# Kernel tuning notes

Hardware: AMD Instinct MI355X
Metric: run time of the kernel (lower is better)

## Reference

```python
import jax, jax.numpy as jnp
import numpy as np

N = 50000
E = 300000
NEG_SLOPE = 0.2
EPS = 1e-16


def setup_inputs() -> dict:
    key = jax.random.key(0)
    ks = jax.random.split(key, 12)
    x = jax.random.normal(ks[0], (N, 27), dtype=jnp.float32)
    edge_index = jax.random.randint(ks[1], (2, E), 0, N, dtype=jnp.int64)
    # layer 1: in=27 -> heads1=4, dim=64
    W1 = jax.random.normal(ks[2], (27, 4 * 64), dtype=jnp.float32) * 0.1
    a_src1 = jax.random.normal(ks[3], (4, 64), dtype=jnp.float32) * 0.1
    a_dst1 = jax.random.normal(ks[4], (4, 64), dtype=jnp.float32) * 0.1
    b1 = jnp.zeros((4 * 64,), dtype=jnp.float32)
    # layer 2: in=256 -> heads2=2, dim=64
    W2 = jax.random.normal(ks[5], (256, 2 * 64), dtype=jnp.float32) * 0.05
    a_src2 = jax.random.normal(ks[6], (2, 64), dtype=jnp.float32) * 0.1
    a_dst2 = jax.random.normal(ks[7], (2, 64), dtype=jnp.float32) * 0.1
    b2 = jnp.zeros((2 * 64,), dtype=jnp.float32)
    # final linear: 128 -> 1
    Wfc = jax.random.normal(ks[8], (128, 1), dtype=jnp.float32) * 0.05
    bfc = jnp.zeros((1,), dtype=jnp.float32)
    return {"x": x, "edge_index": edge_index, "W1": W1, "a_src1": a_src1,
            "a_dst1": a_dst1, "b1": b1, "W2": W2, "a_src2": a_src2,
            "a_dst2": a_dst2, "b2": b2, "Wfc": Wfc, "bfc": bfc}


def gat_layer(x, src, dst, W, a_src, a_dst, b, heads, dim):
    # h: [N, H, D]
    h = (x @ W).reshape(N, heads, dim)
    # per-node attention half-scores: [N, H]
    s_src = jnp.einsum('nhd,hd->nh', h, a_src)
    s_dst = jnp.einsum('nhd,hd->nh', h, a_dst)
    # per-edge logits (gather) + leaky relu: [E', H]
    logits = jax.nn.leaky_relu(s_src[src] + s_dst[dst], negative_slope=NEG_SLOPE)
    # segment softmax over incoming edges at each destination node
    m = jax.ops.segment_max(logits, dst, num_segments=N)  # [N, H]
    m = jnp.where(jnp.isfinite(m), m, 0.0)
    e = jnp.exp(logits - m[dst])
    z = jax.ops.segment_sum(e, dst, num_segments=N)  # [N, H]
    alpha = e / (z[dst] + EPS)
    # weighted scatter-aggregate of source features
    out = jax.ops.segment_sum(h[src] * alpha[:, :, None], dst, num_segments=N)
    return out.reshape(N, heads * dim) + b


def reference(x, edge_index, W1, a_src1, a_dst1, b1, W2, a_src2, a_dst2, b2, Wfc, bfc):
    # add self-loops (PyG GATConv default add_self_loops=True)
    loops = jnp.arange(N, dtype=edge_index.dtype)
    src = jnp.concatenate([edge_index[0], loops])
    dst = jnp.concatenate([edge_index[1], loops])
    h = gat_layer(x, src, dst, W1, a_src1, a_dst1, b1, heads=4, dim=64)
    h = jax.nn.elu(h)
    h = gat_layer(h, src, dst, W2, a_src2, a_dst2, b2, heads=2, dim=64)
    h = jax.nn.elu(h)
    out = h @ Wfc + bfc
    return jax.nn.sigmoid(out)
```

## Files before the change

### kernel.cpp

```cpp
#include <hip/hip_runtime.h>
#include <math.h>

#define N_NODES 50000
#define N_PAD   50016
#define E_EDGES 300000
#define E_TOT   350000
#define NEG 0.2f
#define EPS 1e-16f
#define CAP 32

typedef __attribute__((ext_vector_type(8))) short bf16x8;
typedef __attribute__((ext_vector_type(4))) float f32x4;

__device__ __forceinline__ float leaky(float x) { return x > 0.f ? x : NEG * x; }
__device__ __forceinline__ short f2bf(float v) {
    unsigned u = __float_as_uint(v);
    u += 0x7fffu + ((u >> 16) & 1u);
    return (short)(u >> 16);
}
__device__ __forceinline__ float bflo(unsigned u) { return __uint_as_float(u << 16); }
__device__ __forceinline__ float bfhi(unsigned u) { return __uint_as_float(u & 0xffff0000u); }
__device__ __forceinline__ unsigned bfpack(short a, short b) {
    return (unsigned)(unsigned short)a | ((unsigned)(unsigned short)b << 16);
}

__global__ __launch_bounds__(256) void k_scatter_s1(const int* __restrict__ ei,
        int* __restrict__ cnt, int* __restrict__ eidx,
        const float* __restrict__ x,
        const float* __restrict__ W1, const float* __restrict__ as1,
        const float* __restrict__ ad1, const float* __restrict__ W2,
        float* __restrict__ s1, short* __restrict__ rec,
        short* __restrict__ W1b, short* __restrict__ W2bT) {
    __shared__ float wsvL[216];
    int t = blockIdx.x * 256 + threadIdx.x;
    if (threadIdx.x < 216) {
        int k = threadIdx.x >> 3, j = threadIdx.x & 7;
        const float* av = (j < 4) ? (as1 + j * 64) : (ad1 + (j - 4) * 64);
        const float* wr = W1 + k * 256 + ((j & 3) * 64);
        float s = 0.f;
        #pragma unroll
        for (int d = 0; d < 64; ++d) s += wr[d] * av[d];
        wsvL[threadIdx.x] = s;
    }
    if (t < E_TOT) {
        int s = (t < E_EDGES) ? ei[t] : (t - E_EDGES);
        int d = (t < E_EDGES) ? ei[E_EDGES + t] : (t - E_EDGES);
        int pos = atomicAdd(&cnt[d], 1);
        if (pos < CAP) eidx[d * CAP + pos] = s;
    }
    if (t < 32768) {
        int col = t >> 8, k = t & 255;
        W2bT[t] = f2bf(W2[k * 128 + col]);
    }
    if (t < 8192) {
        int h = t >> 11, col = (t >> 5) & 63, k = t & 31;
        W1b[t] = f2bf(k < 27 ? W1[k * 256 + h * 64 + col] : 0.f);
    }
    __syncthreads();
    if (t < N_NODES * 8) {
        int n = t >> 3, j = t & 7;
        float s = 0.f;
        #pragma unroll
        for (int k = 0; k < 27; ++k) s += x[n * 27 + k] * wsvL[k * 8 + j];
        s1[t] = s;
        if (j < 4) ((float*)rec)[n * 32 + j] = s;
        int c0 = j * 4;
        short p0 = f2bf(c0 + 0 < 27 ? x[n * 27 + c0 + 0] : 0.f);
        short p1 = f2bf(c0 + 1 < 27 ? x[n * 27 + c0 + 1] : 0.f);
        short p2 = f2bf(c0 + 2 < 27 ? x[n * 27 + c0 + 2] : 0.f);
        short p3 = f2bf(c0 + 3 < 27 ? x[n * 27 + c0 + 3] : 0.f);
        uint2 wv;
        wv.x = bfpack(p0, p1);
        wv.y = bfpack(p2, p3);
        *(uint2*)(rec + n * 64 + 8 + c0) = wv;
    }
}

__global__ __launch_bounds__(256) void k_gd(const int* __restrict__ cnt,
        const int* __restrict__ eidx, const short* __restrict__ rec,
        const float* __restrict__ s1, const short* __restrict__ W1b,
        const short* __restrict__ W2bT, const float* __restrict__ b1,
        const float* __restrict__ as2, const float* __restrict__ ad2,
        short* __restrict__ h2b, float* __restrict__ s2) {
    __shared__ short XA[4][32][32];
    __shared__ short O[32 * 264];
    __shared__ float P[4][2][32];
    const float* recf = (const float*)rec;
    int n0 = blockIdx.x * 32;
    f32x4 z4 = {0.f, 0.f, 0.f, 0.f};

    {
        int g = threadIdx.x >> 4;
        int q = threadIdx.x & 15;
        int c2 = 2 * q;
        #pragma unroll
        for (int p = 0; p < 2; ++p) {
            int m = p * 16 + g;
            int n = n0 + m;
            if (n >= N_NODES) {
                *(unsigned*)&XA[0][m][c2] = 0u;
                *(unsigned*)&XA[1][m][c2] = 0u;
                *(unsigned*)&XA[2][m][c2] = 0u;
                *(unsigned*)&XA[3][m][c2] = 0u;
                continue;
            }
            int beg = n * CAP;
            int deg = min(cnt[n], CAP);
            float4 sdv = *(const float4*)(s1 + n * 8 + 4);
            float a0 = 0.f, a1 = 0.f, a2 = 0.f, a3 = 0.f;
            float b0 = 0.f, b1v = 0.f, b2v = 0.f, b3 = 0.f;
            float z0 = 0.f, z1 = 0.f, z2 = 0.f, z3 = 0.f;
            int last = beg + deg - 1;
            for (int i = 0; i < deg; i += 4) {
                bool m1 = (i + 1) < deg, m2 = (i + 2) < deg, m3 = (i + 3) < deg;
                int p0 = beg + i;
                int p1 = m1 ? p0 + 1 : last;
                int p2 = m2 ? p0 + 2 : last;
                int p3 = m3 ? p0 + 3 : last;
                int s0 = eidx[p0];
                int s1i = eidx[p1];
                int s2i = eidx[p2];
                int s3 = eidx[p3];
                float4 sv0 = *(const float4*)(recf + s0 * 32);
                float4 sv1 = *(const float4*)(recf + s1i * 32);
                float4 sv2 = *(const float4*)(recf + s2i * 32);
                float4 sv3 = *(const float4*)(recf + s3 * 32);
                unsigned xv0 = *(const unsigned*)(rec + s0 * 64 + 8 + c2);
                unsigned xv1 = *(const unsigned*)(rec + s1i * 64 + 8 + c2);
                unsigned xv2 = *(const unsigned*)(rec + s2i * 64 + 8 + c2);
                unsigned xv3 = *(const unsigned*)(rec + s3 * 64 + 8 + c2);
                float xa0 = bflo(xv0), xc0 = bfhi(xv0);
                float xa1 = bflo(xv1), xc1 = bfhi(xv1);
                float xa2 = bflo(xv2), xc2 = bfhi(xv2);
                float xa3 = bflo(xv3), xc3 = bfhi(xv3);
                float g1 = m1 ? 1.f : 0.f, g2 = m2 ? 1.f : 0.f, g3 = m3 ? 1.f : 0.f;
                float e00 = __expf(leaky(sv0.x + sdv.x));
                float e01 = __expf(leaky(sv0.y + sdv.y));
                float e02 = __expf(leaky(sv0.z + sdv.z));
                float e03 = __expf(leaky(sv0.w + sdv.w));
                float e10 = g1 * __expf(leaky(sv1.x + sdv.x));
                float e11 = g1 * __expf(leaky(sv1.y + sdv.y));
                float e12 = g1 * __expf(leaky(sv1.z + sdv.z));
                float e13 = g1 * __expf(leaky(sv1.w + sdv.w));
                float e20 = g2 * __expf(leaky(sv2.x + sdv.x));
                float e21 = g2 * __expf(leaky(sv2.y + sdv.y));
                float e22 = g2 * __expf(leaky(sv2.z + sdv.z));
                float e23 = g2 * __expf(leaky(sv2.w + sdv.w));
                float e30 = g3 * __expf(leaky(sv3.x + sdv.x));
                float e31 = g3 * __expf(leaky(sv3.y + sdv.y));
                float e32 = g3 * __expf(leaky(sv3.z + sdv.z));
                float e33 = g3 * __expf(leaky(sv3.w + sdv.w));
                z0 += e00 + e10 + e20 + e30;
                z1 += e01 + e11 + e21 + e31;
                z2 += e02 + e12 + e22 + e32;
                z3 += e03 + e13 + e23 + e33;
                a0 += e00 * xa0 + e10 * xa1 + e20 * xa2 + e30 * xa3;
                a1 += e01 * xa0 + e11 * xa1 + e21 * xa2 + e31 * xa3;
                a2 += e02 * xa0 + e12 * xa1 + e22 * xa2 + e32 * xa3;
                a3 += e03 * xa0 + e13 * xa1 + e23 * xa2 + e33 * xa3;
                b0  += e00 * xc0 + e10 * xc1 + e20 * xc2 + e30 * xc3;
                b1v += e01 * xc0 + e11 * xc1 + e21 * xc2 + e31 * xc3;
                b2v += e02 * xc0 + e12 * xc1 + e22 * xc2 + e32 * xc3;
                b3  += e03 * xc0 + e13 * xc1 + e23 * xc2 + e33 * xc3;
            }
            float i0 = 1.f / (z0 + EPS), i1 = 1.f / (z1 + EPS);
            float i2 = 1.f / (z2 + EPS), i3 = 1.f / (z3 + EPS);
            *(unsigned*)&XA[0][m][c2] = bfpack(f2bf(a0 * i0), f2bf(b0 * i0));
            *(unsigned*)&XA[1][m][c2] = bfpack(f2bf(a1 * i1), f2bf(b1v * i1));
            *(unsigned*)&XA[2][m][c2] = bfpack(f2bf(a2 * i2), f2bf(b2v * i2));
            *(unsigned*)&XA[3][m][c2] = bfpack(f2bf(a3 * i3), f2bf(b3 * i3));
        }
    }
    __syncthreads();

    int w = threadIdx.x >> 6, l = threadIdx.x & 63;
    int lane16 = l & 15, quad = l >> 4;
    {
        bf16x8 am0 = *(const bf16x8*)&XA[w][lane16][quad * 8];
        bf16x8 am1 = *(const bf16x8*)&XA[w][16 + lane16][quad * 8];
        f32x4 c0[4], c1[4];
        #pragma unroll
        for (int nt = 0; nt < 4; ++nt) {
            bf16x8 b = *(const bf16x8*)&W1b[w * 2048 + (nt * 16 + lane16) * 32 + quad * 8];
            c0[nt] = __builtin_amdgcn_mfma_f32_16x16x32_bf16(am0, b, z4, 0, 0, 0);
            c1[nt] = __builtin_amdgcn_mfma_f32_16x16x32_bf16(am1, b, z4, 0, 0, 0);
        }
        #pragma unroll
        for (int nt = 0; nt < 4; ++nt) {
            int col = w * 64 + nt * 16 + lane16;
            float bb = b1[col];
            #pragma unroll
            for (int r2 = 0; r2 < 4; ++r2) {
                float v = c0[nt][r2] + bb;
                v = v > 0.f ? v : __expf(v) - 1.f;
                O[(quad * 4 + r2) * 264 + col] = f2bf(v);
                float u = c1[nt][r2] + bb;
                u = u > 0.f ? u : __expf(u) - 1.f;
                O[(16 + quad * 4 + r2) * 264 + col] = f2bf(u);
            }
        }
    }
    __syncthreads();

    int n0b = n0;
    f32x4 acc[2][2];
    acc[0][0] = z4; acc[0][1] = z4; acc[1][0] = z4; acc[1][1] = z4;
    for (int k0 = 0; k0 < 256; k0 += 32) {
        bf16x8 a0 = *(const bf16x8*)&O[lane16 * 264 + k0 + quad * 8];
        bf16x8 a1 = *(const bf16x8*)&O[(16 + lane16) * 264 + k0 + quad * 8];
        #pragma unroll
        for (int j = 0; j < 2; ++j) {
            int ct = 2 * w + j;
            bf16x8 b2 = *(const bf16x8*)&W2bT[(ct * 16 + lane16) * 256 + k0 + quad * 8];
            acc[0][j] = __builtin_amdgcn_mfma_f32_16x16x32_bf16(a0, b2, acc[0][j], 0, 0, 0);
            acc[1][j] = __builtin_amdgcn_mfma_f32_16x16x32_bf16(a1, b2, acc[1][j], 0, 0, 0);
        }
    }
    float ps[2][4] = {{0.f,0.f,0.f,0.f},{0.f,0.f,0.f,0.f}};
    float pd[2][4] = {{0.f,0.f,0.f,0.f},{0.f,0.f,0.f,0.f}};
    #pragma unroll
    for (int j = 0; j < 2; ++j) {
        int col = (2 * w + j) * 16 + lane16;
        float a_s = as2[col], a_d = ad2[col];
        #pragma unroll
        for (int m = 0; m < 2; ++m) {
            #pragma unroll
            for (int r2 = 0; r2 < 4; ++r2) {
                ps[m][r2] += acc[m][j][r2] * a_s;
                pd[m][r2] += acc[m][j][r2] * a_d;
                int row = n0b + m * 16 + quad * 4 + r2;
                if (row < N_NODES) h2b[row * 128 + col] = f2bf(acc[m][j][r2]);
            }
        }
    }
    #pragma unroll
    for (int off = 1; off <= 8; off <<= 1)
        #pragma unroll
        for (int m = 0; m < 2; ++m)
            #pragma unroll
            for (int r2 = 0; r2 < 4; ++r2) {
                ps[m][r2] += __shfl_xor(ps[m][r2], off);
                pd[m][r2] += __shfl_xor(pd[m][r2], off);
            }
    if (lane16 == 0) {
        #pragma unroll
        for (int m = 0; m < 2; ++m)
            #pragma unroll
            for (int r2 = 0; r2 < 4; ++r2) {
                P[w][0][m * 16 + quad * 4 + r2] = ps[m][r2];
                P[w][1][m * 16 + quad * 4 + r2] = pd[m][r2];
            }
    }
    __syncthreads();
    if (threadIdx.x < 64) {
        int m = threadIdx.x & 31, hd = threadIdx.x >> 5;
        int row = n0b + m;
        if (row < N_NODES) {
            s2[row * 4 + hd]     = P[2 * hd][0][m] + P[2 * hd + 1][0][m];
            s2[row * 4 + 2 + hd] = P[2 * hd][1][m] + P[2 * hd + 1][1][m];
        }
    }
}

__global__ __launch_bounds__(256) void k_agg2_csr(const int* __restrict__ cnt,
        const int* __restrict__ eidx, const float* __restrict__ s2,
        const short* __restrict__ h2b, const float* __restrict__ b2,
        const float* __restrict__ Wfc, const float* __restrict__ bfc,
        float* __restrict__ out) {
    int g = threadIdx.x >> 4;
    int q = threadIdx.x & 15;
    int n = blockIdx.x * 16 + g;
    int beg = n * CAP;
    int deg = min(cnt[n], CAP);
    int h = q >> 3;
    float2 sdv = *(const float2*)(s2 + n * 4 + 2);
    float4 accA = make_float4(0.f, 0.f, 0.f, 0.f);
    float4 accB = make_float4(0.f, 0.f, 0.f, 0.f);
    float z = 0.f;
    float sd = h ? sdv.y : sdv.x;
    int i = 0;
    for (; i + 4 <= deg; i += 4) {
        int a0 = eidx[beg + i], a1 = eidx[beg + i + 1];
        int a2 = eidx[beg + i + 2], a3 = eidx[beg + i + 3];
        float e0 = __expf(leaky(s2[a0 * 4 + h] + sd));
        float e1 = __expf(leaky(s2[a1 * 4 + h] + sd));
        float e2 = __expf(leaky(s2[a2 * 4 + h] + sd));
        float e3 = __expf(leaky(s2[a3 * 4 + h] + sd));
        uint4 v0 = *(const uint4*)(h2b + a0 * 128 + q * 8);
        uint4 v1 = *(const uint4*)(h2b + a1 * 128 + q * 8);
        uint4 v2 = *(const uint4*)(h2b + a2 * 128 + q * 8);
        uint4 v3 = *(const uint4*)(h2b + a3 * 128 + q * 8);
        z += e0 + e1 + e2 + e3;
        accA.x += e0 * bflo(v0.x) + e1 * bflo(v1.x) + e2 * bflo(v2.x) + e3 * bflo(v3.x);
        accA.y += e0 * bfhi(v0.x) + e1 * bfhi(v1.x) + e2 * bfhi(v2.x) + e3 * bfhi(v3.x);
        accA.z += e0 * bflo(v0.y) + e1 * bflo(v1.y) + e2 * bflo(v2.y) + e3 * bflo(v3.y);
        accA.w += e0 * bfhi(v0.y) + e1 * bfhi(v1.y) + e2 * bfhi(v2.y) + e3 * bfhi(v3.y);
        accB.x += e0 * bflo(v0.z) + e1 * bflo(v1.z) + e2 * bflo(v2.z) + e3 * bflo(v3.z);
        accB.y += e0 * bfhi(v0.z) + e1 * bfhi(v1.z) + e2 * bfhi(v2.z) + e3 * bfhi(v3.z);
        accB.z += e0 * bflo(v0.w) + e1 * bflo(v1.w) + e2 * bflo(v2.w) + e3 * bflo(v3.w);
        accB.w += e0 * bfhi(v0.w) + e1 * bfhi(v1.w) + e2 * bfhi(v2.w) + e3 * bfhi(v3.w);
    }
    for (; i < deg; ++i) {
        int a0 = eidx[beg + i];
        float e0 = __expf(leaky(s2[a0 * 4 + h] + sd));
        uint4 v0 = *(const uint4*)(h2b + a0 * 128 + q * 8);
        z += e0;
        accA.x += e0 * bflo(v0.x); accA.y += e0 * bfhi(v0.x);
        accA.z += e0 * bflo(v0.y); accA.w += e0 * bfhi(v0.y);
        accB.x += e0 * bflo(v0.z); accB.y += e0 * bfhi(v0.z);
        accB.z += e0 * bflo(v0.w); accB.w += e0 * bfhi(v0.w);
    }
    float inv = 1.f / (z + EPS);
    int c0 = q * 8;
    float p = 0.f;
    float va[8] = {accA.x, accA.y, accA.z, accA.w, accB.x, accB.y, accB.z, accB.w};
    #pragma unroll
    for (int j = 0; j < 8; ++j) {
        float v = va[j] * inv + b2[c0 + j];
        v = v > 0.f ? v : __expf(v) - 1.f;
        p += v * Wfc[c0 + j];
    }
    #pragma unroll
    for (int off = 1; off <= 8; off <<= 1) p += __shfl_xor(p, off);
    if (q == 0) out[n] = 1.f / (1.f + __expf(-(p + bfc[0])));
}

extern "C" void kernel_launch(void* const* d_in, const int* in_sizes, int n_in,
                              void* d_out, int out_size, void* d_ws, size_t ws_size,
                              hipStream_t stream) {
    const float* x   = (const float*)d_in[0];
    const int*   ei  = (const int*)d_in[1];
    const float* W1  = (const float*)d_in[2];
    const float* as1 = (const float*)d_in[3];
    const float* ad1 = (const float*)d_in[4];
    const float* b1  = (const float*)d_in[5];
    const float* W2  = (const float*)d_in[6];
    const float* as2 = (const float*)d_in[7];
    const float* ad2 = (const float*)d_in[8];
    const float* b2  = (const float*)d_in[9];
    const float* Wfc = (const float*)d_in[10];
    const float* bfc = (const float*)d_in[11];
    float* out = (float*)d_out;

    float* f = (float*)d_ws;
    short* h2b   = (short*)f;
    float* s1    = f + 3200000;
    float* s2    = f + 3600000;
    int*   cnt   = (int*)(f + 3810000);
    int*   eidx  = (int*)(f + 3870000);
    short* W1b   = (short*)(f + 5500000);
    short* W2bT  = (short*)(f + 5510000);
    short* rec   = (short*)(f + 9700000);

    hipMemsetAsync(cnt, 0, N_NODES * sizeof(int), stream);

    k_scatter_s1<<<1563, 256, 0, stream>>>(ei, cnt, eidx, x, W1, as1, ad1, W2,
                                           s1, rec, W1b, W2bT);

    k_gd<<<1563, 256, 0, stream>>>(cnt, eidx, rec, s1, W1b, W2bT, b1,
                                   as2, ad2, h2b, s2);

    k_agg2_csr<<<3125, 256, 0, stream>>>(cnt, eidx, s2, h2b, b2, Wfc, bfc, out);
}
```

Measured before the change: 166.9 us.

## Precompute layer-1 edge exponentials in separate kernel; lane-parallel edge weights in layer-2 aggregation

Result: slower. 171.9 us (+3.0%).

```diff
diff --git a/kernel.cpp b/kernel.cpp
--- a/kernel.cpp
+++ b/kernel.cpp
@@ -76,16 +76,36 @@
     }
 }
 
+__global__ __launch_bounds__(256) void k_edge1(const int* __restrict__ cnt,
+        const int* __restrict__ eidx, const short* __restrict__ rec,
+        const float* __restrict__ s1, float* __restrict__ ealt) {
+    int t = blockIdx.x * 256 + threadIdx.x;
+    int n = t >> 5;
+    int slot = t & 31;
+    int deg = min(cnt[n], CAP);
+    if (slot >= deg) return;
+    int src = eidx[t];
+    const float* recf = (const float*)rec;
+    float4 sv = *(const float4*)(recf + src * 32);
+    float4 sd = *(const float4*)(s1 + n * 8 + 4);
+    float4 e;
+    e.x = __expf(leaky(sv.x + sd.x));
+    e.y = __expf(leaky(sv.y + sd.y));
+    e.z = __expf(leaky(sv.z + sd.z));
+    e.w = __expf(leaky(sv.w + sd.w));
+    *(float4*)(ealt + t * 4) = e;
+}
+
 __global__ __launch_bounds__(256) void k_gd(const int* __restrict__ cnt,
         const int* __restrict__ eidx, const short* __restrict__ rec,
-        const float* __restrict__ s1, const short* __restrict__ W1b,
+        const float* __restrict__ ealt, const short* __restrict__ W1b,
         const short* __restrict__ W2bT, const float* __restrict__ b1,
         const float* __restrict__ as2, const float* __restrict__ ad2,
         short* __restrict__ h2b, float* __restrict__ s2) {
     __shared__ short XA[4][32][32];
     __shared__ short O[32 * 264];
     __shared__ float P[4][2][32];
-    const float* recf = (const float*)rec;
+    const float4* e4 = (const float4*)ealt;
     int n0 = blockIdx.x * 32;
     f32x4 z4 = {0.f, 0.f, 0.f, 0.f};
 
@@ -106,7 +126,6 @@
             }
             int beg = n * CAP;
             int deg = min(cnt[n], CAP);
-            float4 sdv = *(const float4*)(s1 + n * 8 + 4);
             float a0 = 0.f, a1 = 0.f, a2 = 0.f, a3 = 0.f;
             float b0 = 0.f, b1v = 0.f, b2v = 0.f, b3 = 0.f;
             float z0 = 0.f, z1 = 0.f, z2 = 0.f, z3 = 0.f;
@@ -121,10 +140,10 @@
                 int s1i = eidx[p1];
                 int s2i = eidx[p2];
                 int s3 = eidx[p3];
-                float4 sv0 = *(const float4*)(recf + s0 * 32);
-                float4 sv1 = *(const float4*)(recf + s1i * 32);
-                float4 sv2 = *(const float4*)(recf + s2i * 32);
-                float4 sv3 = *(const float4*)(recf + s3 * 32);
+                float4 ev0 = e4[p0];
+                float4 ev1 = e4[p1];
+                float4 ev2 = e4[p2];
+                float4 ev3 = e4[p3];
                 unsigned xv0 = *(const unsigned*)(rec + s0 * 64 + 8 + c2);
                 unsigned xv1 = *(const unsigned*)(rec + s1i * 64 + 8 + c2);
                 unsigned xv2 = *(const unsigned*)(rec + s2i * 64 + 8 + c2);
@@ -134,22 +153,13 @@
                 float xa2 = bflo(xv2), xc2 = bfhi(xv2);
                 float xa3 = bflo(xv3), xc3 = bfhi(xv3);
                 float g1 = m1 ? 1.f : 0.f, g2 = m2 ? 1.f : 0.f, g3 = m3 ? 1.f : 0.f;
-                float e00 = __expf(leaky(sv0.x + sdv.x));
-                float e01 = __expf(leaky(sv0.y + sdv.y));
-                float e02 = __expf(leaky(sv0.z + sdv.z));
-                float e03 = __expf(leaky(sv0.w + sdv.w));
-                float e10 = g1 * __expf(leaky(sv1.x + sdv.x));
-                float e11 = g1 * __expf(leaky(sv1.y + sdv.y));
-                float e12 = g1 * __expf(leaky(sv1.z + sdv.z));
-                float e13 = g1 * __expf(leaky(sv1.w + sdv.w));
-                float e20 = g2 * __expf(leaky(sv2.x + sdv.x));
-                float e21 = g2 * __expf(leaky(sv2.y + sdv.y));
-                float e22 = g2 * __expf(leaky(sv2.z + sdv.z));
-                float e23 = g2 * __expf(leaky(sv2.w + sdv.w));
-                float e30 = g3 * __expf(leaky(sv3.x + sdv.x));
-                float e31 = g3 * __expf(leaky(sv3.y + sdv.y));
-                float e32 = g3 * __expf(leaky(sv3.z + sdv.z));
-                float e33 = g3 * __expf(leaky(sv3.w + sdv.w));
+                float e00 = ev0.x, e01 = ev0.y, e02 = ev0.z, e03 = ev0.w;
+                float e10 = g1 * ev1.x, e11 = g1 * ev1.y;
+                float e12 = g1 * ev1.z, e13 = g1 * ev1.w;
+                float e20 = g2 * ev2.x, e21 = g2 * ev2.y;
+                float e22 = g2 * ev2.z, e23 = g2 * ev2.w;
+                float e30 = g3 * ev3.x, e31 = g3 * ev3.y;
+                float e32 = g3 * ev3.z, e33 = g3 * ev3.w;
                 z0 += e00 + e10 + e20 + e30;
                 z1 += e01 + e11 + e21 + e31;
                 z2 += e02 + e12 + e22 + e32;
@@ -271,44 +281,89 @@
     int q = threadIdx.x & 15;
     int n = blockIdx.x * 16 + g;
     int beg = n * CAP;
+    int espec = eidx[beg + q];
     int deg = min(cnt[n], CAP);
+    int myi = (q < deg) ? espec : n;
     int h = q >> 3;
     float2 sdv = *(const float2*)(s2 + n * 4 + 2);
     float4 accA = make_float4(0.f, 0.f, 0.f, 0.f);
     float4 accB = make_float4(0.f, 0.f, 0.f, 0.f);
     float z = 0.f;
-    float sd = h ? sdv.y : sdv.x;
-    int i = 0;
-    for (; i + 4 <= deg; i += 4) {
-        int a0 = eidx[beg + i], a1 = eidx[beg + i + 1];
-        int a2 = eidx[beg + i + 2], a3 = eidx[beg + i + 3];
-        float e0 = __expf(leaky(s2[a0 * 4 + h] + sd));
-        float e1 = __expf(leaky(s2[a1 * 4 + h] + sd));
-        float e2 = __expf(leaky(s2[a2 * 4 + h] + sd));
-        float e3 = __expf(leaky(s2[a3 * 4 + h] + sd));
-        uint4 v0 = *(const uint4*)(h2b + a0 * 128 + q * 8);
-        uint4 v1 = *(const uint4*)(h2b + a1 * 128 + q * 8);
-        uint4 v2 = *(const uint4*)(h2b + a2 * 128 + q * 8);
-        uint4 v3 = *(const uint4*)(h2b + a3 * 128 + q * 8);
-        z += e0 + e1 + e2 + e3;
-        accA.x += e0 * bflo(v0.x) + e1 * bflo(v1.x) + e2 * bflo(v2.x) + e3 * bflo(v3.x);
-        accA.y += e0 * bfhi(v0.x) + e1 * bfhi(v1.x) + e2 * bfhi(v2.x) + e3 * bfhi(v3.x);
-        accA.z += e0 * bflo(v0.y) + e1 * bflo(v1.y) + e2 * bflo(v2.y) + e3 * bflo(v3.y);
-        accA.w += e0 * bfhi(v0.y) + e1 * bfhi(v1.y) + e2 * bfhi(v2.y) + e3 * bfhi(v3.y);
-        accB.x += e0 * bflo(v0.z) + e1 * bflo(v1.z) + e2 * bflo(v2.z) + e3 * bflo(v3.z);
-        accB.y += e0 * bfhi(v0.z) + e1 * bfhi(v1.z) + e2 * bfhi(v2.z) + e3 * bfhi(v3.z);
-        accB.z += e0 * bflo(v0.w) + e1 * bflo(v1.w) + e2 * bflo(v2.w) + e3 * bflo(v3.w);
-        accB.w += e0 * bfhi(v0.w) + e1 * bfhi(v1.w) + e2 * bfhi(v2.w) + e3 * bfhi(v3.w);
-    }
-    for (; i < deg; ++i) {
-        int a0 = eidx[beg + i];
-        float e0 = __expf(leaky(s2[a0 * 4 + h] + sd));
-        uint4 v0 = *(const uint4*)(h2b + a0 * 128 + q * 8);
-        z += e0;
-        accA.x += e0 * bflo(v0.x); accA.y += e0 * bfhi(v0.x);
-        accA.z += e0 * bflo(v0.y); accA.w += e0 * bfhi(v0.y);
-        accB.x += e0 * bflo(v0.z); accB.y += e0 * bfhi(v0.z);
-        accB.z += e0 * bflo(v0.w); accB.w += e0 * bfhi(v0.w);
+    float2 svq = *(const float2*)(s2 + myi * 4);
+    float mea = __expf(leaky(svq.x + sdv.x));
+    float meb = __expf(leaky(svq.y + sdv.y));
+    int degw = deg;
+    degw = max(degw, __shfl_xor(degw, 16));
+    degw = max(degw, __shfl_xor(degw, 32));
+    if (degw <= 16) {
+        int lw = deg - 1;
+        for (int i = 0; i < degw; i += 4) {
+            bool m0 = i < deg, m1 = (i + 1) < deg;
+            bool m2 = (i + 2) < deg, m3 = (i + 3) < deg;
+            int j0 = m0 ? i : lw;
+            int j1 = m1 ? i + 1 : lw;
+            int j2 = m2 ? i + 2 : lw;
+            int j3 = m3 ? i + 3 : lw;
+            int a0 = __shfl(myi, j0, 16);
+            int a1 = __shfl(myi, j1, 16);
+            int a2 = __shfl(myi, j2, 16);
+            int a3 = __shfl(myi, j3, 16);
+            float ea0 = __shfl(mea, j0, 16), eb0 = __shfl(meb, j0, 16);
+            float ea1 = __shfl(mea, j1, 16), eb1 = __shfl(meb, j1, 16);
+            float ea2 = __shfl(mea, j2, 16), eb2 = __shfl(meb, j2, 16);
+            float ea3 = __shfl(mea, j3, 16), eb3 = __shfl(meb, j3, 16);
+            float e0 = (m0 ? 1.f : 0.f) * (h ? eb0 : ea0);
+            float e1 = (m1 ? 1.f : 0.f) * (h ? eb1 : ea1);
+            float e2 = (m2 ? 1.f : 0.f) * (h ? eb2 : ea2);
+            float e3 = (m3 ? 1.f : 0.f) * (h ? eb3 : ea3);
+            uint4 v0 = *(const uint4*)(h2b + a0 * 128 + q * 8);
+            uint4 v1 = *(const uint4*)(h2b + a1 * 128 + q * 8);
+            uint4 v2 = *(const uint4*)(h2b + a2 * 128 + q * 8);
+            uint4 v3 = *(const uint4*)(h2b + a3 * 128 + q * 8);
+            z += e0 + e1 + e2 + e3;
+            accA.x += e0 * bflo(v0.x) + e1 * bflo(v1.x) + e2 * bflo(v2.x) + e3 * bflo(v3.x);
+            accA.y += e0 * bfhi(v0.x) + e1 * bfhi(v1.x) + e2 * bfhi(v2.x) + e3 * bfhi(v3.x);
+            accA.z += e0 * bflo(v0.y) + e1 * bflo(v1.y) + e2 * bflo(v2.y) + e3 * bflo(v3.y);
+            accA.w += e0 * bfhi(v0.y) + e1 * bfhi(v1.y) + e2 * bfhi(v2.y) + e3 * bfhi(v3.y);
+            accB.x += e0 * bflo(v0.z) + e1 * bflo(v1.z) + e2 * bflo(v2.z) + e3 * bflo(v3.z);
+            accB.y += e0 * bfhi(v0.z) + e1 * bfhi(v1.z) + e2 * bfhi(v2.z) + e3 * bfhi(v3.z);
+            accB.z += e0 * bflo(v0.w) + e1 * bflo(v1.w) + e2 * bflo(v2.w) + e3 * bflo(v3.w);
+            accB.w += e0 * bfhi(v0.w) + e1 * bfhi(v1.w) + e2 * bfhi(v2.w) + e3 * bfhi(v3.w);
+        }
+    } else {
+        float sd = h ? sdv.y : sdv.x;
+        int i = 0;
+        for (; i + 4 <= deg; i += 4) {
+            int a0 = eidx[beg + i], a1 = eidx[beg + i + 1];
+            int a2 = eidx[beg + i + 2], a3 = eidx[beg + i + 3];
+            float e0 = __expf(leaky(s2[a0 * 4 + h] + sd));
+            float e1 = __expf(leaky(s2[a1 * 4 + h] + sd));
+            float e2 = __expf(leaky(s2[a2 * 4 + h] + sd));
+            float e3 = __expf(leaky(s2[a3 * 4 + h] + sd));
+            uint4 v0 = *(const uint4*)(h2b + a0 * 128 + q * 8);
+            uint4 v1 = *(const uint4*)(h2b + a1 * 128 + q * 8);
+            uint4 v2 = *(const uint4*)(h2b + a2 * 128 + q * 8);
+            uint4 v3 = *(const uint4*)(h2b + a3 * 128 + q * 8);
+            z += e0 + e1 + e2 + e3;
+            accA.x += e0 * bflo(v0.x) + e1 * bflo(v1.x) + e2 * bflo(v2.x) + e3 * bflo(v3.x);
+            accA.y += e0 * bfhi(v0.x) + e1 * bfhi(v1.x) + e2 * bfhi(v2.x) + e3 * bfhi(v3.x);
+            accA.z += e0 * bflo(v0.y) + e1 * bflo(v1.y) + e2 * bflo(v2.y) + e3 * bflo(v3.y);
+            accA.w += e0 * bfhi(v0.y) + e1 * bfhi(v1.y) + e2 * bfhi(v2.y) + e3 * bfhi(v3.y);
+            accB.x += e0 * bflo(v0.z) + e1 * bflo(v1.z) + e2 * bflo(v2.z) + e3 * bflo(v3.z);
+            accB.y += e0 * bfhi(v0.z) + e1 * bfhi(v1.z) + e2 * bfhi(v2.z) + e3 * bfhi(v3.z);
+            accB.z += e0 * bflo(v0.w) + e1 * bflo(v1.w) + e2 * bflo(v2.w) + e3 * bflo(v3.w);
+            accB.w += e0 * bfhi(v0.w) + e1 * bfhi(v1.w) + e2 * bfhi(v2.w) + e3 * bfhi(v3.w);
+        }
+        for (; i < deg; ++i) {
+            int a0 = eidx[beg + i];
+            float e0 = __expf(leaky(s2[a0 * 4 + h] + sd));
+            uint4 v0 = *(const uint4*)(h2b + a0 * 128 + q * 8);
+            z += e0;
+            accA.x += e0 * bflo(v0.x); accA.y += e0 * bfhi(v0.x);
+            accA.z += e0 * bflo(v0.y); accA.w += e0 * bfhi(v0.y);
+            accB.x += e0 * bflo(v0.z); accB.y += e0 * bfhi(v0.z);
+            accB.z += e0 * bflo(v0.w); accB.w += e0 * bfhi(v0.w);
+        }
     }
     float inv = 1.f / (z + EPS);
     int c0 = q * 8;
@@ -351,13 +406,16 @@
     short* W1b   = (short*)(f + 5500000);
     short* W2bT  = (short*)(f + 5510000);
     short* rec   = (short*)(f + 9700000);
+    float* ealt  = f + 11400000;
 
     hipMemsetAsync(cnt, 0, N_NODES * sizeof(int), stream);
 
     k_scatter_s1<<<1563, 256, 0, stream>>>(ei, cnt, eidx, x, W1, as1, ad1, W2,
                                            s1, rec, W1b, W2bT);
 
-    k_gd<<<1563, 256, 0, stream>>>(cnt, eidx, rec, s1, W1b, W2bT, b1,
+    k_edge1<<<6250, 256, 0, stream>>>(cnt, eidx, rec, s1, ealt);
+
+    k_gd<<<1563, 256, 0, stream>>>(cnt, eidx, rec, ealt, W1b, W2bT, b1,
                                    as2, ad2, h2b, s2);
 
     k_agg2_csr<<<3125, 256, 0, stream>>>(cnt, eidx, s2, h2b, b2, Wfc, bfc, out);
```
